# Performance work log

Hardware: AMD Instinct MI355X
Metric: run time of the kernel (lower is better)

Reference implementation:

```python
import jax, jax.numpy as jnp
import numpy as np

EPS = 1e-12  # F.normalize eps


def qweight(r, i, j, k):
    # Hamilton-product block matrix: (out, in, kh, kw) from 4 blocks of (out//4, in//4, kh, kw)
    row_r = jnp.concatenate([r, -i, -j, -k], axis=1)
    row_i = jnp.concatenate([i, r, -k, j], axis=1)
    row_j = jnp.concatenate([j, k, r, -i], axis=1)
    row_k = jnp.concatenate([k, -j, i, r], axis=1)
    return jnp.concatenate([row_r, row_i, row_j, row_k], axis=0)


def qconv(x, r, i, j, k, b, stride, pad):
    w = qweight(r, i, j, k)
    y = jax.lax.conv_general_dilated(
        x, w, window_strides=(stride, stride),
        padding=[(pad, pad), (pad, pad)],
        dimension_numbers=('NCHW', 'OIHW', 'NCHW'))
    return y + b[None, :, None, None]


def setup_inputs() -> dict:
    key = jax.random.key(0)
    ks = jax.random.split(key, 16)
    dim, heads, B, H, W = 128, 4, 2, 128, 128
    d4 = dim // 4
    std = 0.02
    inp = {
        'x': jax.random.normal(ks[0], (B, dim, H, W), jnp.float32),
        'qkv_r': jax.random.normal(ks[1], (3 * d4, d4, 1, 1), jnp.float32) * std,
        'qkv_i': jax.random.normal(ks[2], (3 * d4, d4, 1, 1), jnp.float32) * std,
        'qkv_j': jax.random.normal(ks[3], (3 * d4, d4, 1, 1), jnp.float32) * std,
        'qkv_k': jax.random.normal(ks[4], (3 * d4, d4, 1, 1), jnp.float32) * std,
        'qkv_b': jnp.zeros((3 * dim,), jnp.float32),
        'dw_r': jax.random.normal(ks[5], (3 * d4, 3 * d4, 3, 3), jnp.float32) * std,
        'dw_i': jax.random.normal(ks[6], (3 * d4, 3 * d4, 3, 3), jnp.float32) * std,
        'dw_j': jax.random.normal(ks[7], (3 * d4, 3 * d4, 3, 3), jnp.float32) * std,
        'dw_k': jax.random.normal(ks[8], (3 * d4, 3 * d4, 3, 3), jnp.float32) * std,
        'dw_b': jnp.zeros((3 * dim,), jnp.float32),
        'po_r': jax.random.normal(ks[9], (d4, d4, 1, 1), jnp.float32) * std,
        'po_i': jax.random.normal(ks[10], (d4, d4, 1, 1), jnp.float32) * std,
        'po_j': jax.random.normal(ks[11], (d4, d4, 1, 1), jnp.float32) * std,
        'po_k': jax.random.normal(ks[12], (d4, d4, 1, 1), jnp.float32) * std,
        'po_b': jnp.zeros((dim,), jnp.float32),
        'temperature': jnp.ones((heads, 1, 1), jnp.float32),
    }
    return inp


def reference(x, qkv_r, qkv_i, qkv_j, qkv_k, qkv_b,
              dw_r, dw_i, dw_j, dw_k, dw_b,
              po_r, po_i, po_j, po_k, po_b, temperature):
    b, c, h, w = x.shape
    heads = temperature.shape[0]
    ch = c // heads  # channels per head

    qkv = qconv(x, qkv_r, qkv_i, qkv_j, qkv_k, qkv_b, 1, 0)
    qkv = qconv(qkv, dw_r, dw_i, dw_j, dw_k, dw_b, 1, 1)
    q, k, v = jnp.split(qkv, 3, axis=1)

    def to_heads(t):  # b (head c) h w -> b head c (h w)
        return t.reshape(b, heads, ch, h * w)

    q, k, v = to_heads(q), to_heads(k), to_heads(v)
    # L2-normalize along spatial axis (torch F.normalize semantics)
    q = q / jnp.maximum(jnp.linalg.norm(q, axis=-1, keepdims=True), EPS)
    k = k / jnp.maximum(jnp.linalg.norm(k, axis=-1, keepdims=True), EPS)

    attn = jnp.einsum('bhcs,bhds->bhcd', q, k) * temperature[None]
    attn = jax.nn.softmax(attn, axis=-1)
    out = jnp.einsum('bhcd,bhds->bhcs', attn, v)

    out = out.reshape(b, c, h, w)
    out = qconv(out, po_r, po_i, po_j, po_k, po_b, 1, 0)
    return out
```

## Files before the change

kernel.cpp:

```cpp
#include <hip/hip_runtime.h>
#include <hip/hip_bf16.h>
#include <string.h>

typedef __hip_bfloat16 bf16;
typedef __bf16 bf16x8 __attribute__((ext_vector_type(8)));
typedef float f32x4 __attribute__((ext_vector_type(4)));

typedef __attribute__((address_space(1))) void* gas_ptr;
typedef __attribute__((address_space(3))) void* las_ptr;

__device__ __forceinline__ void gload_lds16(const void* g, void* l) {
  __builtin_amdgcn_global_load_lds((gas_ptr)(void*)g, (las_ptr)l, 16, 0, 0);
}


__device__ __forceinline__ void qexpand(const float* r, const float* i_, const float* j_,
                                        const float* k_, bf16* dst, int O4, int I4, int taps,
                                        int gid) {
  int C = 4 * I4;
  int o   = gid / (taps * C);
  int rem = gid % (taps * C);
  int tap = rem / C, c = rem % C;
  int br = o / O4, orr = o % O4, bc = c / I4, ic = c % I4;
  const float* srcs[4] = { r, i_, j_, k_ };
  const int   comp[4][4] = { {0,1,2,3}, {1,0,3,2}, {2,3,0,1}, {3,2,1,0} };
  const float sgn [4][4] = { {1,-1,-1,-1}, {1,1,-1,1}, {1,1,1,-1}, {1,-1,1,1} };
  float v = srcs[comp[br][bc]][(size_t)(orr * I4 + ic) * taps + tap];
  dst[gid] = __float2bfloat16(v * sgn[br][bc]);
}

#define N_W1 49152
#define N_W2 1327104
#define N_W3 16384
#define N_BR 396288
#define N_MI 900
#define N_SQ 512
#define N_SR 8192
#define N_PREP (N_W1 + N_W2 + N_W3 + N_BR + N_MI + N_SQ + N_SR)

__global__ void prep(const float* __restrict__ qr, const float* __restrict__ qi,
                     const float* __restrict__ qj, const float* __restrict__ qk,
                     const float* __restrict__ dr, const float* __restrict__ di,
                     const float* __restrict__ dj, const float* __restrict__ dk,
                     const float* __restrict__ pr, const float* __restrict__ pi,
                     const float* __restrict__ pj, const float* __restrict__ pk,
                     const float* __restrict__ qb, const float* __restrict__ db,
                     const float* __restrict__ pb, const float* __restrict__ tp,
                     bf16* __restrict__ W1t, bf16* __restrict__ W2t, bf16* __restrict__ W3t,
                     bf16* __restrict__ q1p, float* __restrict__ misc,
                     float* __restrict__ ssq, float* __restrict__ Sraw) {
  int gid = blockIdx.x * 256 + threadIdx.x;
  if (gid < N_W1) { qexpand(qr, qi, qj, qk, W1t, 96, 32, 1, gid); return; }
  gid -= N_W1;
  if (gid < N_W2) { qexpand(dr, di, dj, dk, W2t, 96, 96, 9, gid); return; }
  gid -= N_W2;
  if (gid < N_W3) { qexpand(pr, pi, pj, pk, W3t, 32, 32, 1, gid); return; }
  gid -= N_W3;
  if (gid < N_BR) {
    int b = gid / (516 * 384);
    int rem = gid % (516 * 384);
    int cell = rem / 384, c = rem % 384;
    int hp, wp;
    if      (cell < 130) { hp = 0;   wp = cell; }
    else if (cell < 260) { hp = 129; wp = cell - 130; }
    else if (cell < 388) { hp = cell - 260 + 1; wp = 0; }
    else                 { hp = cell - 388 + 1; wp = 129; }
    q1p[((size_t)((b * 130 + hp) * 130) + wp) * 384 + c] = __float2bfloat16(0.0f);
    return;
  }
  gid -= N_BR;
  if (gid < N_MI) {
    if (gid < 384)      misc[gid] = qb[gid];
    else if (gid < 768) misc[gid] = db[gid - 384];
    else if (gid < 896) misc[gid] = pb[gid - 768];
    else                misc[gid] = tp[gid - 896];
    return;
  }
  gid -= N_MI;
  if (gid < N_SQ) { ssq[gid] = 0.0f; return; }
  gid -= N_SQ;
  if (gid < N_SR) { Sraw[gid] = 0.0f; return; }
}

__global__ __launch_bounds__(256) void gemm_qkv1f(const float* __restrict__ x,
                                                  const bf16* __restrict__ wt,
                                                  const float* __restrict__ bias,
                                                  bf16* __restrict__ out) {
  __shared__ __align__(16) bf16 Axl[4 * 64 * 32];
  __shared__ __align__(16) bf16 Bl [4 * 128 * 32];
  const int h = blockIdx.x, wh = blockIdx.y, b = blockIdx.z;
  const int tid = threadIdx.x, wid = tid >> 6, lane = tid & 63;
  const int l16 = lane & 15, q = lane >> 4;
  const int sq8 = (q ^ ((l16 >> 1) & 3)) * 8;
  const int wm = (wid & 1) * 32, wn = (wid >> 1) * 64;
  {
    const int c = tid >> 1, seg = tid & 1;
    const float* src = x + ((size_t)(b * 128 + c) << 14) + h * 128 + wh * 64 + seg * 32;
    const int cb = (c >> 5) * 2048, c31 = c & 31;
    for (int j = 0; j < 8; ++j) {
      float4 v = *(const float4*)(src + j * 4);
      int w0 = seg * 32 + j * 4;
      float vv[4] = { v.x, v.y, v.z, v.w };
      for (int r = 0; r < 4; ++r) {
        int w = w0 + r;
        Axl[cb + w * 32 + (c31 ^ ((((w >> 1) & 3)) << 3))] = __float2bfloat16(vv[r]);
      }
    }
  }
  for (int ot = 0; ot < 3; ++ot) {
    __syncthreads();
    const bf16* bbase = wt + (size_t)ot * 16384;
    for (int i = 0; i < 8; ++i) {
      int ci = wid * 512 + i * 64 + lane;
      int chunk = ci >> 9, rem = ci & 511;
      int o = rem >> 2, part = rem & 3;
      int ps = part ^ ((o >> 1) & 3);
      gload_lds16(bbase + o * 128 + chunk * 32 + ps * 8, Bl + (size_t)(wid * 512 + i * 64) * 8);
    }
    __syncthreads();
    f32x4 acc[2][4] = {};
    for (int k = 0; k < 4; ++k) {
      bf16x8 af[2], bfr[4];
      for (int mi = 0; mi < 2; ++mi)
        af[mi] = *(const bf16x8*)&Axl[k * 2048 + (wm + mi * 16 + l16) * 32 + sq8];
      for (int ni = 0; ni < 4; ++ni)
        bfr[ni] = *(const bf16x8*)&Bl[k * 4096 + (wn + ni * 16 + l16) * 32 + sq8];
      for (int mi = 0; mi < 2; ++mi)
        for (int ni = 0; ni < 4; ++ni)
          acc[mi][ni] = __builtin_amdgcn_mfma_f32_16x16x32_bf16(af[mi], bfr[ni], acc[mi][ni], 0, 0, 0);
    }
    for (int ni = 0; ni < 4; ++ni) {
      int o = ot * 128 + wn + ni * 16 + l16;
      float bv = bias[o];
      for (int mi = 0; mi < 2; ++mi) {
        int w0 = wh * 64 + wm + mi * 16 + q * 4;
        for (int r = 0; r < 4; ++r) {
          int w = w0 + r;
          size_t idx = ((size_t)((b * 130 + h + 1) * 130) + (w + 1)) * 384 + o;
          out[idx] = __float2bfloat16(acc[mi][ni][r] + bv);
        }
      }
    }
    __syncthreads();
  }
}

__global__ __launch_bounds__(256, 2) void conv3x3(const bf16* __restrict__ in,
                                                  const bf16* __restrict__ wt,
                                                  const float* __restrict__ bias,
                                                  bf16* __restrict__ out) {
  __shared__ __align__(16) short Al[6 * 132 * 32];
  __shared__ __align__(16) short Bl[9 * 48 * 32];
  const int lid = blockIdx.x;
  const int xcd = lid & 7, slot = lid >> 3;
  const int b = xcd & 1;
  const int h0 = (xcd >> 1) * 32 + (slot & 7) * 4;
  const int ob = (slot >> 3) * 48;
  const int tid = threadIdx.x, wid = tid >> 6, lane = tid & 63;
  const int l16 = lane & 15, q = lane >> 4;
  const int sA[3] = { (q ^ (((l16 + 0) >> 1) & 3)) * 8,
                      (q ^ (((l16 + 1) >> 1) & 3)) * 8,
                      (q ^ (((l16 + 2) >> 1) & 3)) * 8 };
  const int sB = sA[0];
  f32x4 acc[8][3] = {};
  const bf16* abase = in + (size_t)b * 130 * 130 * 384;
  const bf16* bbase = wt + (size_t)ob * 3456;
  for (int c0 = 0; c0 < 384; c0 += 32) {
    __syncthreads();
    for (int i = 0; i < 12; ++i) {
      int g = wid * 792 + i * 64;
      int ci = g + lane;
      int row = ci / 528, rem = ci % 528;
      int w = rem >> 2, part = rem & 3;
      int ps = part ^ ((w >> 1) & 3);
      gload_lds16(abase + ((size_t)(h0 + row) * 130 + w) * 384 + c0 + ps * 8, &Al[g * 8]);
    }
    if (lane < 24) {
      int g = wid * 792 + 768;
      int ci = g + lane;
      int row = ci / 528, rem = ci % 528;
      int w = rem >> 2, part = rem & 3;
      int ps = part ^ ((w >> 1) & 3);
      gload_lds16(abase + ((size_t)(h0 + row) * 130 + w) * 384 + c0 + ps * 8, &Al[g * 8]);
    }
    for (int i = 0; i < 6; ++i) {
      int g = wid * 432 + i * 64;
      int ci = g + lane;
      int tap = ci / 192, rem = ci % 192;
      int o = rem >> 2, part = rem & 3;
      int ps = part ^ ((o >> 1) & 3);
      gload_lds16(bbase + (size_t)o * 3456 + tap * 384 + c0 + ps * 8, &Bl[g * 8]);
    }
    if (lane < 48) {
      int g = wid * 432 + 384;
      int ci = g + lane;
      int tap = ci / 192, rem = ci % 192;
      int o = rem >> 2, part = rem & 3;
      int ps = part ^ ((o >> 1) & 3);
      gload_lds16(bbase + (size_t)o * 3456 + tap * 384 + c0 + ps * 8, &Bl[g * 8]);
    }
    __syncthreads();
    for (int dh = 0; dh < 3; ++dh)
      for (int dw = 0; dw < 3; ++dw) {
        bf16x8 af[8], bfr[3];
        for (int mi = 0; mi < 8; ++mi)
          af[mi] = *(const bf16x8*)&Al[((wid + dh) * 132 + mi * 16 + l16 + dw) * 32 + sA[dw]];
        for (int ni = 0; ni < 3; ++ni)
          bfr[ni] = *(const bf16x8*)&Bl[((dh * 3 + dw) * 48 + ni * 16 + l16) * 32 + sB];
        for (int mi = 0; mi < 8; ++mi)
          for (int ni = 0; ni < 3; ++ni)
            acc[mi][ni] = __builtin_amdgcn_mfma_f32_16x16x32_bf16(af[mi], bfr[ni], acc[mi][ni], 0, 0, 0);
      }
  }
  const int h = h0 + wid;
  for (int ni = 0; ni < 3; ++ni) {
    int o = ob + ni * 16 + l16;
    float bv = bias[o];
    for (int mi = 0; mi < 8; ++mi) {
      int w0 = mi * 16 + q * 4;
      for (int r = 0; r < 4; ++r) {
        int w = w0 + r;
        out[((size_t)(b * 16384 + h * 128 + w)) * 384 + o] = __float2bfloat16(acc[mi][ni][r] + bv);
      }
    }
  }
}

__global__ __launch_bounds__(256) void attn_qk(const bf16* __restrict__ q2,
                                               float* __restrict__ Sraw,
                                               float* __restrict__ ssq) {
  const int sc = blockIdx.x, h = blockIdx.y, b = blockIdx.z;
  const int t = threadIdx.x;
  __shared__ bf16 qt[64][32];
  __shared__ bf16 kt[64][32];
  __shared__ float Sl[1024];
  __shared__ float nql[32], nkl[32];
  for (int i = t; i < 1024; i += 256) Sl[i] = 0.0f;
  if (t < 32) nql[t] = 0.0f;
  else if (t < 64) nkl[t - 32] = 0.0f;
  const int slq = t >> 2, seg = t & 3;
  const int slot = t & 63, sg = t >> 6;
  const int cg = (slot & 7) * 4, dg = (slot >> 3) * 4;
  float acc[4][4] = {};
  float sq[4] = {}, sk[4] = {};
  for (int it = 0; it < 8; ++it) {
    int sbase = sc * 512 + it * 64;
    __syncthreads();
    {
      size_t rq = ((size_t)(b * 16384 + sbase + slq)) * 384 + h * 32 + seg * 8;
      *(bf16x8*)&qt[slq][seg * 8] = *(const bf16x8*)&q2[rq];
      *(bf16x8*)&kt[slq][seg * 8] = *(const bf16x8*)&q2[rq + 128];
    }
    __syncthreads();
    for (int sl = sg * 16; sl < sg * 16 + 16; ++sl) {
      float qv[4], kv[4];
      for (int a = 0; a < 4; ++a) qv[a] = __bfloat162float(qt[sl][cg + a]);
      for (int d = 0; d < 4; ++d) kv[d] = __bfloat162float(kt[sl][dg + d]);
      if (dg == 0) for (int a = 0; a < 4; ++a) sq[a] += qv[a] * qv[a];
      if (cg == 0) for (int d = 0; d < 4; ++d) sk[d] += kv[d] * kv[d];
      for (int a = 0; a < 4; ++a)
        for (int d = 0; d < 4; ++d) acc[a][d] += qv[a] * kv[d];
    }
  }
  for (int a = 0; a < 4; ++a)
    for (int d = 0; d < 4; ++d)
      atomicAdd(&Sl[(cg + a) * 32 + dg + d], acc[a][d]);
  if (dg == 0) for (int a = 0; a < 4; ++a) atomicAdd(&nql[cg + a], sq[a]);
  if (cg == 0) for (int d = 0; d < 4; ++d) atomicAdd(&nkl[dg + d], sk[d]);
  __syncthreads();
  float* Sg = Sraw + (size_t)((b * 4 + h) * 1024);
  for (int i = t * 4; i < t * 4 + 4; ++i) atomicAdd(&Sg[i], Sl[i]);
  if (t < 32) atomicAdd(&ssq[b * 256 + h * 32 + t], nql[t]);
  else if (t < 64) atomicAdd(&ssq[b * 256 + 128 + h * 32 + (t - 32)], nkl[t - 32]);
}

__global__ __launch_bounds__(256) void attn_out(const bf16* __restrict__ q2,
                                                const float* __restrict__ Sraw,
                                                const float* __restrict__ ssq,
                                                const float* __restrict__ misc,
                                                const bf16* __restrict__ w3,
                                                float* __restrict__ out) {
  __shared__ __align__(16) bf16 Ml[4 * 128 * 32];
  __shared__ float Pl[4][32][32];
  __shared__ __align__(16) short Bl[128 * 32];
  __shared__ float rqa[128], rka[128];
  const int tile = blockIdx.x;
  const int b = tile >> 7, s0 = (tile & 127) * 128;
  const int t = threadIdx.x;
  const int wid = t >> 6, lane = t & 63;
  const int l16 = lane & 15, q = lane >> 4;
  const int sq8 = (q ^ ((l16 >> 1) & 3)) * 8;
  {
    float v = ssq[b * 256 + t];
    float rv = 1.0f / fmaxf(sqrtf(fmaxf(v, 0.0f)), 1e-12f);
    if (t < 128) rqa[t] = rv; else rka[t - 128] = rv;
  }
  __syncthreads();
  if (t < 128) {
    int hh = t >> 5, c = t & 31;
    const float* Sr = Sraw + ((size_t)((b * 4 + hh) * 32 + c)) * 32;
    float tv = misc[896 + hh];
    float rq = rqa[t];
    float row[32];
    float m = -1e30f;
    for (int d = 0; d < 32; ++d) { row[d] = Sr[d] * tv * rq * rka[hh * 32 + d]; m = fmaxf(m, row[d]); }
    float sum = 0.0f;
    for (int d = 0; d < 32; ++d) { row[d] = expf(row[d] - m); sum += row[d]; }
    float inv = 1.0f / sum;
    for (int d = 0; d < 32; ++d) Pl[hh][c][d] = row[d] * inv;
  }
  __syncthreads();
  {
    const int o = t >> 1, half = t & 1;
    const int sw = ((o >> 1) & 3) << 3;
    for (int hh2 = 0; hh2 < 2; ++hh2) {
      int hv = half * 2 + hh2;
      float w3r[32];
      const bf16* wrow = w3 + o * 128 + hv * 32;
      for (int c = 0; c < 32; ++c) w3r[c] = __bfloat162float(wrow[c]);
      for (int d = 0; d < 32; ++d) {
        float s = 0.0f;
        for (int c = 0; c < 32; ++c) s += w3r[c] * Pl[hv][c][d];
        Ml[hv * 4096 + o * 32 + (d ^ sw)] = __float2bfloat16(s);
      }
    }
  }
  f32x4 acc[4][4] = {};
  const int wmo = (wid & 1) * 64, wns = (wid >> 1) * 64;
  for (int kc = 0; kc < 4; ++kc) {
    __syncthreads();
    for (int i = 0; i < 2; ++i) {
      int ci = i * 256 + t;
      int s = ci >> 2, part = ci & 3;
      int ps = part ^ ((s >> 1) & 3);
      gload_lds16(q2 + ((size_t)(b * 16384 + s0 + s)) * 384 + 256 + kc * 32 + ps * 8,
                  &Bl[(size_t)(i * 256 + wid * 64) * 8]);
    }
    __syncthreads();
    bf16x8 af[4], bfr[4];
    for (int mi = 0; mi < 4; ++mi)
      af[mi] = *(const bf16x8*)&Ml[kc * 4096 + (wmo + mi * 16 + l16) * 32 + sq8];
    for (int ni = 0; ni < 4; ++ni)
      bfr[ni] = *(const bf16x8*)&Bl[(wns + ni * 16 + l16) * 32 + sq8];
    for (int mi = 0; mi < 4; ++mi)
      for (int ni = 0; ni < 4; ++ni)
        acc[mi][ni] = __builtin_amdgcn_mfma_f32_16x16x32_bf16(af[mi], bfr[ni], acc[mi][ni], 0, 0, 0);
  }
  for (int ni = 0; ni < 4; ++ni) {
    int s = s0 + wns + ni * 16 + l16;
    for (int mi = 0; mi < 4; ++mi) {
      int o0 = wmo + mi * 16 + q * 4;
      for (int r = 0; r < 4; ++r) {
        int o = o0 + r;
        out[(size_t)b * 2097152 + (size_t)o * 16384 + s] = acc[mi][ni][r] + misc[768 + o];
      }
    }
  }
}

extern "C" void kernel_launch(void* const* d_in, const int* in_sizes, int n_in,
                              void* d_out, int out_size, void* d_ws, size_t ws_size,
                              hipStream_t stream) {
  const float* x     = (const float*)d_in[0];
  const float* qkv_r = (const float*)d_in[1];
  const float* qkv_i = (const float*)d_in[2];
  const float* qkv_j = (const float*)d_in[3];
  const float* qkv_k = (const float*)d_in[4];
  const float* qkv_b = (const float*)d_in[5];
  const float* dw_r  = (const float*)d_in[6];
  const float* dw_i  = (const float*)d_in[7];
  const float* dw_j  = (const float*)d_in[8];
  const float* dw_k  = (const float*)d_in[9];
  const float* dw_b  = (const float*)d_in[10];
  const float* po_r  = (const float*)d_in[11];
  const float* po_i  = (const float*)d_in[12];
  const float* po_j  = (const float*)d_in[13];
  const float* po_k  = (const float*)d_in[14];
  const float* po_b  = (const float*)d_in[15];
  const float* temp  = (const float*)d_in[16];

  char* ws = (char*)d_ws;
  size_t off = 0;
  auto alloc = [&](size_t bytes) { char* p = ws + off; off += (bytes + 255) & ~(size_t)255; return p; };
  bf16* q1p  = (bf16*)alloc((size_t)2 * 130 * 130 * 384 * 2);
  bf16* q2   = (bf16*)alloc((size_t)2 * 16384 * 384 * 2);
  bf16* W1t  = (bf16*)alloc((size_t)384 * 128 * 2);
  bf16* W2t  = (bf16*)alloc((size_t)384 * 3456 * 2);
  bf16* W3t  = (bf16*)alloc((size_t)128 * 128 * 2);
  float* ssq  = (float*)alloc((size_t)2 * 256 * 4);
  float* Sraw = (float*)alloc((size_t)2 * 4 * 32 * 32 * 4);
  float* misc = (float*)alloc((size_t)900 * 4);

  prep<<<(N_PREP + 255) / 256, 256, 0, stream>>>(qkv_r, qkv_i, qkv_j, qkv_k,
                                                 dw_r, dw_i, dw_j, dw_k,
                                                 po_r, po_i, po_j, po_k,
                                                 qkv_b, dw_b, po_b, temp,
                                                 W1t, W2t, W3t, q1p, misc, ssq, Sraw);
  gemm_qkv1f<<<dim3(128, 2, 2), 256, 0, stream>>>(x, W1t, misc, q1p);
  conv3x3<<<512, 256, 0, stream>>>(q1p, W2t, misc + 384, q2);
  attn_qk<<<dim3(32, 4, 2), 256, 0, stream>>>(q2, Sraw, ssq);
  attn_out<<<256, 256, 0, stream>>>(q2, Sraw, ssq, misc, W3t, (float*)d_out);
}
```

Before: 226.4 us.

## Compute QK^T Gram and norms with MFMA on swizzled transposed LDS tile

Rewrites the attn_qk kernel so the whole 512-position chunk of q and k is loaded at once, transposed in registers and stored to LDS with an XOR swizzle. The 32x32 Gram matrix is then built with bf16 MFMA instructions instead of scalar FMAs. Squared norms come from the diagonal of q·q and k·k MFMAs. This removes the scalar inner loop and the repeated per-iteration barriers, at the cost of a larger LDS footprint (64 KB) that may limit occupancy, plus wasted MFMA work on the norm products.

New measurement: 217.7 us. -3.8%, faster.

```diff
diff --git a/kernel.cpp b/kernel.cpp
--- a/kernel.cpp
+++ b/kernel.cpp
@@ -231,42 +231,74 @@
                                                float* __restrict__ ssq) {
   const int sc = blockIdx.x, h = blockIdx.y, b = blockIdx.z;
   const int t = threadIdx.x;
-  __shared__ bf16 qt[64][32];
-  __shared__ bf16 kt[64][32];
+  __shared__ __align__(16) short qkT[64 * 512];
   __shared__ float Sl[1024];
   __shared__ float nql[32], nkl[32];
   for (int i = t; i < 1024; i += 256) Sl[i] = 0.0f;
   if (t < 32) nql[t] = 0.0f;
   else if (t < 64) nkl[t - 32] = 0.0f;
-  const int slq = t >> 2, seg = t & 3;
-  const int slot = t & 63, sg = t >> 6;
-  const int cg = (slot & 7) * 4, dg = (slot >> 3) * 4;
-  float acc[4][4] = {};
-  float sq[4] = {}, sk[4] = {};
-  for (int it = 0; it < 8; ++it) {
-    int sbase = sc * 512 + it * 64;
-    __syncthreads();
-    {
-      size_t rq = ((size_t)(b * 16384 + sbase + slq)) * 384 + h * 32 + seg * 8;
-      *(bf16x8*)&qt[slq][seg * 8] = *(const bf16x8*)&q2[rq];
-      *(bf16x8*)&kt[slq][seg * 8] = *(const bf16x8*)&q2[rq + 128];
-    }
-    __syncthreads();
-    for (int sl = sg * 16; sl < sg * 16 + 16; ++sl) {
-      float qv[4], kv[4];
-      for (int a = 0; a < 4; ++a) qv[a] = __bfloat162float(qt[sl][cg + a]);
-      for (int d = 0; d < 4; ++d) kv[d] = __bfloat162float(kt[sl][dg + d]);
-      if (dg == 0) for (int a = 0; a < 4; ++a) sq[a] += qv[a] * qv[a];
-      if (cg == 0) for (int d = 0; d < 4; ++d) sk[d] += kv[d] * kv[d];
-      for (int a = 0; a < 4; ++a)
-        for (int d = 0; d < 4; ++d) acc[a][d] += qv[a] * kv[d];
-    }
-  }
-  for (int a = 0; a < 4; ++a)
-    for (int d = 0; d < 4; ++d)
-      atomicAdd(&Sl[(cg + a) * 32 + dg + d], acc[a][d]);
-  if (dg == 0) for (int a = 0; a < 4; ++a) atomicAdd(&nql[cg + a], sq[a]);
-  if (cg == 0) for (int d = 0; d < 4; ++d) atomicAdd(&nkl[dg + d], sk[d]);
+  const int ch8 = t & 7, sg = t >> 3;
+  const int goff = (ch8 < 4) ? (h * 32 + ch8 * 8) : (128 + h * 32 + (ch8 - 4) * 8);
+  const int S0 = sc * 512;
+  for (int p = 0; p < 2; ++p) {
+    int schunk = sg + p * 32;
+    const bf16* src = q2 + (size_t)(b * 16384 + S0 + schunk * 8) * 384 + goff;
+    bf16x8 ld[8];
+#pragma unroll
+    for (int s = 0; s < 8; ++s) ld[s] = *(const bf16x8*)(src + (size_t)s * 384);
+#pragma unroll
+    for (int j = 0; j < 8; ++j) {
+      bf16x8 wv;
+#pragma unroll
+      for (int s = 0; s < 8; ++s) wv[s] = ld[s][j];
+      int row = ch8 * 8 + j;
+      int sw = (row ^ (row >> 3)) & 7;
+      *(bf16x8*)&qkT[row * 512 + (schunk ^ sw) * 8] = wv;
+    }
+  }
+  __syncthreads();
+  const int wid = t >> 6, lane = t & 63;
+  const int l16 = lane & 15, q = lane >> 4;
+  f32x4 Sacc[2][2] = {};
+  f32x4 qqa[2] = {}, kka[2] = {};
+  for (int it = 0; it < 4; ++it) {
+    int chunkR = wid * 16 + it * 4 + q;
+    bf16x8 afq[2], afk[2];
+#pragma unroll
+    for (int ct = 0; ct < 2; ++ct) {
+      int rq = ct * 16 + l16;
+      afq[ct] = *(const bf16x8*)&qkT[rq * 512 + (chunkR ^ ((rq ^ (rq >> 3)) & 7)) * 8];
+      int rk = 32 + ct * 16 + l16;
+      afk[ct] = *(const bf16x8*)&qkT[rk * 512 + (chunkR ^ ((rk ^ (rk >> 3)) & 7)) * 8];
+    }
+#pragma unroll
+    for (int ct = 0; ct < 2; ++ct)
+#pragma unroll
+      for (int dt = 0; dt < 2; ++dt)
+        Sacc[ct][dt] = __builtin_amdgcn_mfma_f32_16x16x32_bf16(afq[ct], afk[dt], Sacc[ct][dt], 0, 0, 0);
+#pragma unroll
+    for (int ct = 0; ct < 2; ++ct) {
+      qqa[ct] = __builtin_amdgcn_mfma_f32_16x16x32_bf16(afq[ct], afq[ct], qqa[ct], 0, 0, 0);
+      kka[ct] = __builtin_amdgcn_mfma_f32_16x16x32_bf16(afk[ct], afk[ct], kka[ct], 0, 0, 0);
+    }
+  }
+#pragma unroll
+  for (int ct = 0; ct < 2; ++ct)
+#pragma unroll
+    for (int dt = 0; dt < 2; ++dt)
+#pragma unroll
+      for (int r = 0; r < 4; ++r)
+        atomicAdd(&Sl[(ct * 16 + q * 4 + r) * 32 + dt * 16 + l16], Sacc[ct][dt][r]);
+  if ((l16 >> 2) == q) {
+    int r = l16 & 3;
+#pragma unroll
+    for (int ct = 0; ct < 2; ++ct) {
+      float vq = r == 0 ? qqa[ct][0] : r == 1 ? qqa[ct][1] : r == 2 ? qqa[ct][2] : qqa[ct][3];
+      float vk = r == 0 ? kka[ct][0] : r == 1 ? kka[ct][1] : r == 2 ? kka[ct][2] : kka[ct][3];
+      atomicAdd(&nql[ct * 16 + l16], vq);
+      atomicAdd(&nkl[ct * 16 + l16], vk);
+    }
+  }
   __syncthreads();
   float* Sg = Sraw + (size_t)((b * 4 + h) * 1024);
   for (int i = t * 4; i < t * 4 + 4; ++i) atomicAdd(&Sg[i], Sl[i]);
```
